# Performance work log

Measured on AMD Instinct MI355X. Metric: run time of the kernel, lower is better.

## Reference

```python
import jax, jax.numpy as jnp
import numpy as np

N = 16_777_216  # total elements
B = 16_384      # number of segments (graphs/batches)
EPS = 1e-12


def setup_inputs() -> dict:
    key = jax.random.key(0)
    k1, k2, k3 = jax.random.split(key, 3)
    preds = jax.random.normal(k1, (N,), dtype=jnp.float32)
    target = jax.random.normal(k2, (N,), dtype=jnp.float32)
    batch_map = jnp.sort(jax.random.randint(k3, (N,), 0, B, dtype=jnp.int64))
    return {"preds": preds, "target": target, "batch_map": batch_map}


def reference(preds, target, batch_map):
    # per-segment squared norms and dot product (three scatter-sums in torch)
    seg = lambda v: jax.ops.segment_sum(v, batch_map, num_segments=B,
                                        indices_are_sorted=True)
    preds_norm = jnp.sqrt(seg(preds * preds))      # [B]
    target_norm = jnp.sqrt(seg(target * target))   # [B]
    dot_product = seg(preds * target)              # [B]
    cosine = dot_product / jnp.maximum(preds_norm * target_norm, EPS)
    return jnp.mean(1.0 - cosine)
```

## Files before the change

kernel.cpp:

```cpp
#include <hip/hip_runtime.h>

#define NSEG 16384
#define EPS 1e-12f

__global__ void bsearch_kernel(const int* __restrict__ map,
                               int* __restrict__ start, int n) {
    int b = blockIdx.x * blockDim.x + threadIdx.x;
    if (b > NSEG) return;
    int lo = 0, hi = n;
    while (lo < hi) {
        int mid = (lo + hi) >> 1;
        if (map[mid] < b) lo = mid + 1; else hi = mid;
    }
    start[b] = lo;
}

__global__ void seg_cos_kernel(const float* __restrict__ p,
                               const float* __restrict__ t,
                               const int* __restrict__ start,
                               float* __restrict__ loss) {
    const int wid  = threadIdx.x >> 6;
    const int lane = threadIdx.x & 63;
    const int seg  = blockIdx.x * (blockDim.x >> 6) + wid;
    if (seg >= NSEG) return;

    const int s0 = start[seg];
    const int s1 = start[seg + 1];

    float a = 0.0f, b = 0.0f, c = 0.0f;

    const int a0 = (s0 + 3) & ~3;
    const int a1 = s1 & ~3;

    if (a1 <= a0) {
        for (int i = s0 + lane; i < s1; i += 64) {
            float pv = p[i], tv = t[i];
            a += pv * pv; b += tv * tv; c += pv * tv;
        }
    } else {
        int i = s0 + lane;
        if (i < a0) {
            float pv = p[i], tv = t[i];
            a += pv * pv; b += tv * tv; c += pv * tv;
        }
        i = a1 + lane;
        if (i < s1) {
            float pv = p[i], tv = t[i];
            a += pv * pv; b += tv * tv; c += pv * tv;
        }
        const float4* p4 = (const float4*)p;
        const float4* t4 = (const float4*)t;
        const int v0 = a0 >> 2, v1 = a1 >> 2;
        for (int v = v0 + lane; v < v1; v += 64) {
            float4 pv = p4[v], tv = t4[v];
            a += pv.x * pv.x + pv.y * pv.y + pv.z * pv.z + pv.w * pv.w;
            b += tv.x * tv.x + tv.y * tv.y + tv.z * tv.z + tv.w * tv.w;
            c += pv.x * tv.x + pv.y * tv.y + pv.z * tv.z + pv.w * tv.w;
        }
    }

    #pragma unroll
    for (int off = 32; off > 0; off >>= 1) {
        a += __shfl_down(a, off);
        b += __shfl_down(b, off);
        c += __shfl_down(c, off);
    }

    if (lane == 0) {
        float denom = sqrtf(a) * sqrtf(b);
        float cosv = c / fmaxf(denom, EPS);
        loss[seg] = 1.0f - cosv;
    }
}

__global__ void finalize_kernel(const float* __restrict__ loss,
                                float* __restrict__ out) {
    float local = 0.0f;
    for (int i = threadIdx.x; i < NSEG; i += blockDim.x)
        local += loss[i];
    #pragma unroll
    for (int off = 32; off > 0; off >>= 1)
        local += __shfl_down(local, off);

    __shared__ float wsum[16];
    int wid = threadIdx.x >> 6;
    if ((threadIdx.x & 63) == 0) wsum[wid] = local;
    __syncthreads();
    if (threadIdx.x == 0) {
        float tot = 0.0f;
        int nw = blockDim.x >> 6;
        for (int w = 0; w < nw; ++w) tot += wsum[w];
        out[0] = tot / (float)NSEG;
    }
}

extern "C" void kernel_launch(void* const* d_in, const int* in_sizes, int n_in,
                              void* d_out, int out_size, void* d_ws, size_t ws_size,
                              hipStream_t stream) {
    const float* p = (const float*)d_in[0];
    const float* t = (const float*)d_in[1];
    const int*   s = (const int*)d_in[2];
    int n = in_sizes[0];

    int*   start = (int*)d_ws;
    float* loss  = (float*)(start + NSEG + 2);

    bsearch_kernel<<<(NSEG + 1 + 255) / 256, 256, 0, stream>>>(s, start, n);

    seg_cos_kernel<<<NSEG / 4, 256, 0, stream>>>(p, t, start, loss);

    finalize_kernel<<<1, 1024, 0, stream>>>(loss, (float*)d_out);
}
```

Baseline: 41.00 us.

## Fuse segment-boundary binary search into cosine kernel and unroll vector loads

Removes the separate binary-search kernel: each wavefront's first two lanes compute the segment start and end directly and broadcast them by shuffle, which saves one launch and the workspace round trip. The float4 accumulation loop is unrolled four times so more loads are in flight per lane, and the finalize kernel reads the per-segment losses as float4. The cost is that the binary-search latency now sits on the critical path of every wavefront before it can stream data, and two lanes per segment search where there used to be one.

```diff
diff --git a/kernel.cpp b/kernel.cpp
--- a/kernel.cpp
+++ b/kernel.cpp
@@ -3,29 +3,29 @@
 #define NSEG 16384
 #define EPS 1e-12f
 
-__global__ void bsearch_kernel(const int* __restrict__ map,
-                               int* __restrict__ start, int n) {
-    int b = blockIdx.x * blockDim.x + threadIdx.x;
-    if (b > NSEG) return;
+__device__ __forceinline__ int lower_bound(const int* __restrict__ map,
+                                           int n, int b) {
     int lo = 0, hi = n;
     while (lo < hi) {
         int mid = (lo + hi) >> 1;
         if (map[mid] < b) lo = mid + 1; else hi = mid;
     }
-    start[b] = lo;
+    return lo;
 }
 
-__global__ void seg_cos_kernel(const float* __restrict__ p,
-                               const float* __restrict__ t,
-                               const int* __restrict__ start,
-                               float* __restrict__ loss) {
+__global__ void seg_cos_fused(const float* __restrict__ p,
+                              const float* __restrict__ t,
+                              const int* __restrict__ map,
+                              float* __restrict__ loss, int n) {
     const int wid  = threadIdx.x >> 6;
     const int lane = threadIdx.x & 63;
     const int seg  = blockIdx.x * (blockDim.x >> 6) + wid;
     if (seg >= NSEG) return;
 
-    const int s0 = start[seg];
-    const int s1 = start[seg + 1];
+    int bound = 0;
+    if (lane < 2) bound = lower_bound(map, n, seg + lane);
+    const int s0 = __shfl(bound, 0);
+    const int s1 = __shfl(bound, 1);
 
     float a = 0.0f, b = 0.0f, c = 0.0f;
 
@@ -50,12 +50,31 @@
         }
         const float4* p4 = (const float4*)p;
         const float4* t4 = (const float4*)t;
-        const int v0 = a0 >> 2, v1 = a1 >> 2;
-        for (int v = v0 + lane; v < v1; v += 64) {
+        const int v1 = a1 >> 2;
+        int v = (a0 >> 2) + lane;
+        for (; v + 192 < v1; v += 256) {
+            float4 p0 = p4[v],       t0 = t4[v];
+            float4 p1 = p4[v + 64],  t1 = t4[v + 64];
+            float4 p2 = p4[v + 128], t2 = t4[v + 128];
+            float4 p3 = p4[v + 192], t3 = t4[v + 192];
+            a += p0.x*p0.x + p0.y*p0.y + p0.z*p0.z + p0.w*p0.w;
+            b += t0.x*t0.x + t0.y*t0.y + t0.z*t0.z + t0.w*t0.w;
+            c += p0.x*t0.x + p0.y*t0.y + p0.z*t0.z + p0.w*t0.w;
+            a += p1.x*p1.x + p1.y*p1.y + p1.z*p1.z + p1.w*p1.w;
+            b += t1.x*t1.x + t1.y*t1.y + t1.z*t1.z + t1.w*t1.w;
+            c += p1.x*t1.x + p1.y*t1.y + p1.z*t1.z + p1.w*t1.w;
+            a += p2.x*p2.x + p2.y*p2.y + p2.z*p2.z + p2.w*p2.w;
+            b += t2.x*t2.x + t2.y*t2.y + t2.z*t2.z + t2.w*t2.w;
+            c += p2.x*t2.x + p2.y*t2.y + p2.z*t2.z + p2.w*t2.w;
+            a += p3.x*p3.x + p3.y*p3.y + p3.z*p3.z + p3.w*p3.w;
+            b += t3.x*t3.x + t3.y*t3.y + t3.z*t3.z + t3.w*t3.w;
+            c += p3.x*t3.x + p3.y*t3.y + p3.z*t3.z + p3.w*t3.w;
+        }
+        for (; v < v1; v += 64) {
             float4 pv = p4[v], tv = t4[v];
-            a += pv.x * pv.x + pv.y * pv.y + pv.z * pv.z + pv.w * pv.w;
-            b += tv.x * tv.x + tv.y * tv.y + tv.z * tv.z + tv.w * tv.w;
-            c += pv.x * tv.x + pv.y * tv.y + pv.z * tv.z + pv.w * tv.w;
+            a += pv.x*pv.x + pv.y*pv.y + pv.z*pv.z + pv.w*pv.w;
+            b += tv.x*tv.x + tv.y*tv.y + tv.z*tv.z + tv.w*tv.w;
+            c += pv.x*tv.x + pv.y*tv.y + pv.z*tv.z + pv.w*tv.w;
         }
     }
 
@@ -73,11 +92,13 @@
     }
 }
 
-__global__ void finalize_kernel(const float* __restrict__ loss,
+__global__ void finalize_kernel(const float4* __restrict__ loss4,
                                 float* __restrict__ out) {
     float local = 0.0f;
-    for (int i = threadIdx.x; i < NSEG; i += blockDim.x)
-        local += loss[i];
+    for (int i = threadIdx.x; i < NSEG / 4; i += blockDim.x) {
+        float4 v = loss4[i];
+        local += v.x + v.y + v.z + v.w;
+    }
     #pragma unroll
     for (int off = 32; off > 0; off >>= 1)
         local += __shfl_down(local, off);
@@ -102,12 +123,8 @@
     const int*   s = (const int*)d_in[2];
     int n = in_sizes[0];
 
-    int*   start = (int*)d_ws;
-    float* loss  = (float*)(start + NSEG + 2);
+    float* loss = (float*)d_ws;
 
-    bsearch_kernel<<<(NSEG + 1 + 255) / 256, 256, 0, stream>>>(s, start, n);
-
-    seg_cos_kernel<<<NSEG / 4, 256, 0, stream>>>(p, t, start, loss);
-
-    finalize_kernel<<<1, 1024, 0, stream>>>(loss, (float*)d_out);
+    seg_cos_fused<<<NSEG / 4, 256, 0, stream>>>(p, t, s, loss, n);
+    finalize_kernel<<<1, 1024, 0, stream>>>((const float4*)loss, (float*)d_out);
 }
```

After: 41.87 us. 2.1% more time.
